# Performance work log

Hardware: AMD Instinct MI355X
Metric: run time of the kernel (lower is better)

Reference implementation:

```python
import jax, jax.numpy as jnp
import numpy as np

B, T, U = 8, 200, 100
D_ENC = D_DEC = J = 512
V = 1024


def setup_inputs() -> dict:
    key = jax.random.key(0)
    ks = jax.random.split(key, 7)
    s = 0.02
    return {
        "enc_out": jax.random.normal(ks[0], (B, T, 1, D_ENC), jnp.float32),
        "dec_out": jax.random.normal(ks[1], (B, 1, U, D_DEC), jnp.float32),
        "W_enc": jax.random.normal(ks[2], (J, D_ENC), jnp.float32) * s,
        "b_enc": jax.random.normal(ks[3], (J,), jnp.float32) * s,
        "W_dec": jax.random.normal(ks[4], (J, D_DEC), jnp.float32) * s,
        "W_out": jax.random.normal(ks[5], (V, J), jnp.float32) * s,
        "b_out": jax.random.normal(ks[6], (V,), jnp.float32) * s,
    }


def reference(enc_out, dec_out, W_enc, b_enc, W_dec, W_out, b_out):
    # lin_enc: (B,T,1,J); lin_dec (no bias): (B,1,U,J)
    enc_proj = jnp.einsum('btod,jd->btoj', enc_out, W_enc) + b_enc
    dec_proj = jnp.einsum('boud,jd->bouj', dec_out, W_dec)
    # broadcast add -> (B,T,U,J), tanh activation
    joint = jnp.tanh(enc_proj + dec_proj)
    # lin_out -> (B,T,U,V)
    return jnp.einsum('btuj,vj->btuv', joint, W_out) + b_out
```

## Files before the change

kernel.cpp:

```cpp
#include <hip/hip_runtime.h>


#define B_ 8
#define T_ 200
#define U_ 100
#define J_ 512
#define V_ 1024
#define M2_ (B_ * T_ * U_)

typedef __attribute__((ext_vector_type(4))) float float4v;
typedef __attribute__((ext_vector_type(8))) short short8;
typedef __attribute__((ext_vector_type(4))) float f32x4;

#define DEV static __device__ __forceinline__

DEV unsigned short f2bf(float f) {
  unsigned int u = __float_as_uint(f);
  u += 0x7FFFu + ((u >> 16) & 1u);
  return (unsigned short)(u >> 16);
}

DEV short8 pack8(float4v a, float4v b) {
  short8 r;
  r[0] = (short)f2bf(a[0]); r[1] = (short)f2bf(a[1]);
  r[2] = (short)f2bf(a[2]); r[3] = (short)f2bf(a[3]);
  r[4] = (short)f2bf(b[0]); r[5] = (short)f2bf(b[1]);
  r[6] = (short)f2bf(b[2]); r[7] = (short)f2bf(b[3]);
  return r;
}

DEV float fast_tanh(float x) {
  float t = __expf(2.0f * x);
  float r = __builtin_amdgcn_rcpf(t + 1.0f);
  return __builtin_fmaf(-2.0f, r, 1.0f);
}

__global__ __launch_bounds__(256) void convert_wout(
    const float* __restrict__ W, unsigned short* __restrict__ Wb) {
  int i = blockIdx.x * 256 + threadIdx.x;
  const float* p = W + (size_t)i * 8;
  float4v a = *(const float4v*)p;
  float4v b = *(const float4v*)(p + 4);
  *(short8*)(Wb + (size_t)i * 8) = pack8(a, b);
}

#define SWZ64(base, row, kb) ((base) + ((row) << 7) + ((((kb) ^ ((row) & 7))) << 4))

__global__ __launch_bounds__(256) void proj_kernel(
    const float* __restrict__ enc_out, const float* __restrict__ dec_out,
    const float* __restrict__ W_enc, const float* __restrict__ b_enc,
    const float* __restrict__ W_dec,
    float* __restrict__ enc_proj, float* __restrict__ dec_proj) {
  __shared__ char lds[16384];
  char* Albs = lds;
  char* Blbs = lds + 8192;

  int bid = blockIdx.x;
  bool is_enc = bid < 200;
  const float* srcA;
  const float* Wsrc;
  float* dst;
  int Mrows, bm, bn;
  if (is_enc) {
    bm = bid >> 3; bn = bid & 7;
    srcA = enc_out; Wsrc = W_enc; dst = enc_proj; Mrows = 1600;
  } else {
    int q = bid - 200;
    bm = q >> 3; bn = q & 7;
    srcA = dec_out; Wsrc = W_dec; dst = dec_proj; Mrows = 800;
  }

  int t = threadIdx.x;
  int l = t & 63;
  int w = t >> 6;
  int wrow = w >> 1, wcol = w & 1;

  f32x4 acc[2][2] = {};

  for (int k0 = 0; k0 < 512; k0 += 64) {
#pragma unroll
    for (int i = 0; i < 2; ++i) {
      int g = t + i * 256;
      int row = g >> 3, kb = g & 7;
      int arow = bm * 64 + row;
      if (arow >= Mrows) arow = Mrows - 1;
      const float* pa = srcA + (size_t)arow * 512 + k0 + kb * 8;
      *(short8*)SWZ64(Albs, row, kb) =
          pack8(*(const float4v*)pa, *(const float4v*)(pa + 4));
      const float* pb = Wsrc + (size_t)(bn * 64 + row) * 512 + k0 + kb * 8;
      *(short8*)SWZ64(Blbs, row, kb) =
          pack8(*(const float4v*)pb, *(const float4v*)(pb + 4));
    }
    __syncthreads();
#pragma unroll
    for (int h = 0; h < 2; ++h) {
      int kb = h * 4 + (l >> 4);
      short8 af[2], bfv[2];
#pragma unroll
      for (int m = 0; m < 2; ++m) {
        int row = wrow * 32 + m * 16 + (l & 15);
        af[m] = *(const short8*)SWZ64(Albs, row, kb);
      }
#pragma unroll
      for (int n = 0; n < 2; ++n) {
        int row = wcol * 32 + n * 16 + (l & 15);
        bfv[n] = *(const short8*)SWZ64(Blbs, row, kb);
      }
#pragma unroll
      for (int m = 0; m < 2; ++m)
#pragma unroll
        for (int n = 0; n < 2; ++n)
          acc[m][n] = __builtin_amdgcn_mfma_f32_16x16x32_bf16(
              af[m], bfv[n], acc[m][n], 0, 0, 0);
    }
    __syncthreads();
  }

#pragma unroll
  for (int n = 0; n < 2; ++n) {
    int col = bn * 64 + wcol * 32 + n * 16 + (l & 15);
    float bias = is_enc ? b_enc[col] : 0.0f;
#pragma unroll
    for (int m = 0; m < 2; ++m) {
#pragma unroll
      for (int j = 0; j < 4; ++j) {
        int gr = bm * 64 + wrow * 32 + m * 16 + (l >> 4) * 4 + j;
        if (gr < Mrows) dst[(size_t)gr * 512 + col] = acc[m][n][j] + bias;
      }
    }
  }
}

__global__ __launch_bounds__(512) void joint_kernel(
    const float* __restrict__ enc_proj, const float* __restrict__ dec_proj,
    const unsigned short* __restrict__ Wb, const float* __restrict__ b_out,
    float* __restrict__ out) {
  __shared__ char lds[163840];
  char* Astrip = lds;
  char* Bbuf0 = lds + 131072;
  char* Bbuf1 = lds + 131072 + 16384;

  int bm = blockIdx.x;
  int t = threadIdx.x;
  int l = t & 63;
  int w = t >> 6;
  int wrow = w >> 2;
  int wcol = w & 3;

  {
#pragma unroll
    for (int i = 0; i < 2; ++i) {
      int g = t + i * 512;
      int rowc = g >> 3;
      int kbp = g & 7;
      int kb = kbp ^ (rowc & 7);
      const unsigned short* src = Wb + (size_t)rowc * 512 + kb * 8;
      __builtin_amdgcn_global_load_lds(
          (const __attribute__((address_space(1))) unsigned int*)src,
          (__attribute__((address_space(3))) unsigned int*)(Bbuf0 + g * 16),
          16, 0, 0);
    }
  }

  {
    int row = t >> 2;
    int gr = bm * 128 + row;
    int b_ = gr / 20000;
    int rem = gr - b_ * 20000;
    int u_ = rem % 100;
    int erow = gr / 100;
    int drow = b_ * 100 + u_;
    const float* pe_base = enc_proj + (size_t)erow * 512;
    const float* pd_base = dec_proj + (size_t)drow * 512;
    char* arow_base = Astrip + row * 1024;
    int swz = row & 7;
#pragma unroll
    for (int i = 0; i < 16; ++i) {
      int kb = i * 4 + (t & 3);
      const float* pe = pe_base + kb * 8;
      const float* pd = pd_base + kb * 8;
      float4v e0 = *(const float4v*)pe;
      float4v e1 = *(const float4v*)(pe + 4);
      float4v d0 = *(const float4v*)pd;
      float4v d1 = *(const float4v*)(pd + 4);
      float4v j0, j1;
#pragma unroll
      for (int q = 0; q < 4; ++q) {
        j0[q] = fast_tanh(e0[q] + d0[q]);
        j1[q] = fast_tanh(e1[q] + d1[q]);
      }
      *(short8*)(arow_base + ((kb ^ swz) << 4)) = pack8(j0, j1);
    }
  }
  __syncthreads();

  f32x4 acc[4][2] = {{{0.f,0.f,0.f,0.f}}};
#pragma unroll
  for (int m = 0; m < 4; ++m)
#pragma unroll
    for (int n = 0; n < 2; ++n)
      acc[m][n] = (f32x4){0.f, 0.f, 0.f, 0.f};

  for (int s = 0; s < 64; ++s) {
    char* Bcur = (s & 1) ? Bbuf1 : Bbuf0;
    char* Bnxt = (s & 1) ? Bbuf0 : Bbuf1;

    if (s < 63) {
      int nt1 = (s + 1) >> 3;
      int k01 = ((s + 1) & 7) * 64;
#pragma unroll
      for (int i = 0; i < 2; ++i) {
        int g = t + i * 512;
        int rowc = g >> 3;
        int kbp = g & 7;
        int kb = kbp ^ (rowc & 7);
        const unsigned short* src =
            Wb + (size_t)(nt1 * 128 + rowc) * 512 + k01 + kb * 8;
        __builtin_amdgcn_global_load_lds(
            (const __attribute__((address_space(1))) unsigned int*)src,
            (__attribute__((address_space(3))) unsigned int*)(Bnxt + g * 16),
            16, 0, 0);
      }
    }

    int k0g = (s & 7) * 8;
#pragma unroll
    for (int kk = 0; kk < 2; ++kk) {
      short8 af[4], bfv[2];
      int kbA = k0g + kk * 4 + (l >> 4);
#pragma unroll
      for (int m = 0; m < 4; ++m) {
        int r = wrow * 64 + m * 16 + (l & 15);
        af[m] = *(const short8*)(Astrip + r * 1024 + (((kbA ^ (r & 7))) << 4));
      }
      int kbB = kk * 4 + (l >> 4);
#pragma unroll
      for (int n = 0; n < 2; ++n) {
        int rc = wcol * 32 + n * 16 + (l & 15);
        bfv[n] = *(const short8*)(Bcur + rc * 128 + (((kbB ^ (rc & 7))) << 4));
      }
      __builtin_amdgcn_s_setprio(1);
#pragma unroll
      for (int m = 0; m < 4; ++m)
#pragma unroll
        for (int n = 0; n < 2; ++n)
          acc[m][n] = __builtin_amdgcn_mfma_f32_16x16x32_bf16(
              af[m], bfv[n], acc[m][n], 0, 0, 0);
      __builtin_amdgcn_s_setprio(0);
    }

    if ((s & 7) == 7) {
      int nt = s >> 3;
#pragma unroll
      for (int n = 0; n < 2; ++n) {
        int col = nt * 128 + wcol * 32 + n * 16 + (l & 15);
        float bias = b_out[col];
#pragma unroll
        for (int m = 0; m < 4; ++m) {
          int r0 = bm * 128 + wrow * 64 + m * 16 + (l >> 4) * 4;
#pragma unroll
          for (int j = 0; j < 4; ++j)
            out[(size_t)(r0 + j) * 1024 + col] = acc[m][n][j] + bias;
          acc[m][n] = (f32x4){0.f, 0.f, 0.f, 0.f};
        }
      }
    }

    __syncthreads();
  }
}

extern "C" void kernel_launch(void* const* d_in, const int* in_sizes, int n_in,
                              void* d_out, int out_size, void* d_ws, size_t ws_size,
                              hipStream_t stream) {
  const float* enc_out = (const float*)d_in[0];
  const float* dec_out = (const float*)d_in[1];
  const float* W_enc   = (const float*)d_in[2];
  const float* b_enc   = (const float*)d_in[3];
  const float* W_dec   = (const float*)d_in[4];
  const float* W_out   = (const float*)d_in[5];
  const float* b_out   = (const float*)d_in[6];
  float* out = (float*)d_out;

  char* ws = (char*)d_ws;
  float* enc_proj = (float*)ws;
  float* dec_proj = (float*)(ws + 3276800);
  unsigned short* Wb = (unsigned short*)(ws + 3276800 + 1638400);

  hipLaunchKernelGGL(convert_wout, dim3(256), dim3(256), 0, stream, W_out, Wb);
  hipLaunchKernelGGL(proj_kernel, dim3(304), dim3(256), 0, stream,
                     enc_out, dec_out, W_enc, b_enc, W_dec, enc_proj, dec_proj);
  hipLaunchKernelGGL(joint_kernel, dim3(M2_ / 128), dim3(512), 0, stream,
                     enc_proj, dec_proj, Wb, b_out, out);
}
```

Baseline: 856.7 us.

## Read W_out fragments directly from global in k-group-major layout, drop LDS B staging

The W_out conversion now writes bf16 weights in a k-group-major layout so each MFMA B fragment is one contiguous 16-byte global load. The joint kernel no longer stages B tiles through double-buffered LDS with per-step barriers. Each wave instead computes a 64x64 tile (4x4 MFMAs) over four column passes, reading B straight from global/L2. The A strip uses an unswizzled k-group-major LDS layout and LDS shrinks to 128KB, with launch_bounds(512,2) added. The intent is to remove barrier and LDS-copy overhead and raise per-wave MFMA density, at the risk of global-load latency stalls and LDS bank conflicts on A reads.

Measured after the change: 839.2 us. -2.0%, faster.

```diff
diff --git a/kernel.cpp b/kernel.cpp
--- a/kernel.cpp
+++ b/kernel.cpp
@@ -36,12 +36,14 @@
 }
 
 __global__ __launch_bounds__(256) void convert_wout(
-    const float* __restrict__ W, unsigned short* __restrict__ Wb) {
+    const float* __restrict__ W, unsigned short* __restrict__ Wbt) {
   int i = blockIdx.x * 256 + threadIdx.x;
-  const float* p = W + (size_t)i * 8;
+  int col = i & 1023;
+  int g = i >> 10;
+  const float* p = W + (size_t)col * 512 + g * 8;
   float4v a = *(const float4v*)p;
   float4v b = *(const float4v*)(p + 4);
-  *(short8*)(Wb + (size_t)i * 8) = pack8(a, b);
+  *(short8*)(Wbt + (size_t)g * 8192 + col * 8) = pack8(a, b);
 }
 
 #define SWZ64(base, row, kb) ((base) + ((row) << 7) + ((((kb) ^ ((row) & 7))) << 4))
@@ -131,14 +133,11 @@
   }
 }
 
-__global__ __launch_bounds__(512) void joint_kernel(
+__global__ __launch_bounds__(512, 2) void joint_kernel(
     const float* __restrict__ enc_proj, const float* __restrict__ dec_proj,
-    const unsigned short* __restrict__ Wb, const float* __restrict__ b_out,
+    const unsigned short* __restrict__ Wbt, const float* __restrict__ b_out,
     float* __restrict__ out) {
-  __shared__ char lds[163840];
-  char* Astrip = lds;
-  char* Bbuf0 = lds + 131072;
-  char* Bbuf1 = lds + 131072 + 16384;
+  __shared__ char As[131072];
 
   int bm = blockIdx.x;
   int t = threadIdx.x;
@@ -146,24 +145,12 @@
   int w = t >> 6;
   int wrow = w >> 2;
   int wcol = w & 3;
+  int lr = l & 15;
+  int lg = l >> 4;
 
   {
-#pragma unroll
-    for (int i = 0; i < 2; ++i) {
-      int g = t + i * 512;
-      int rowc = g >> 3;
-      int kbp = g & 7;
-      int kb = kbp ^ (rowc & 7);
-      const unsigned short* src = Wb + (size_t)rowc * 512 + kb * 8;
-      __builtin_amdgcn_global_load_lds(
-          (const __attribute__((address_space(1))) unsigned int*)src,
-          (__attribute__((address_space(3))) unsigned int*)(Bbuf0 + g * 16),
-          16, 0, 0);
-    }
-  }
-
-  {
-    int row = t >> 2;
+    int row = t & 127;
+    int gbase = t >> 7;
     int gr = bm * 128 + row;
     int b_ = gr / 20000;
     int rem = gr - b_ * 20000;
@@ -172,13 +159,11 @@
     int drow = b_ * 100 + u_;
     const float* pe_base = enc_proj + (size_t)erow * 512;
     const float* pd_base = dec_proj + (size_t)drow * 512;
-    char* arow_base = Astrip + row * 1024;
-    int swz = row & 7;
 #pragma unroll
     for (int i = 0; i < 16; ++i) {
-      int kb = i * 4 + (t & 3);
-      const float* pe = pe_base + kb * 8;
-      const float* pd = pd_base + kb * 8;
+      int g = gbase + i * 4;
+      const float* pe = pe_base + g * 8;
+      const float* pd = pd_base + g * 8;
       float4v e0 = *(const float4v*)pe;
       float4v e1 = *(const float4v*)(pe + 4);
       float4v d0 = *(const float4v*)pd;
@@ -189,84 +174,62 @@
         j0[q] = fast_tanh(e0[q] + d0[q]);
         j1[q] = fast_tanh(e1[q] + d1[q]);
       }
-      *(short8*)(arow_base + ((kb ^ swz) << 4)) = pack8(j0, j1);
+      *(short8*)(As + g * 2048 + row * 16) = pack8(j0, j1);
     }
   }
   __syncthreads();
 
-  f32x4 acc[4][2] = {{{0.f,0.f,0.f,0.f}}};
-#pragma unroll
-  for (int m = 0; m < 4; ++m)
-#pragma unroll
-    for (int n = 0; n < 2; ++n)
-      acc[m][n] = (f32x4){0.f, 0.f, 0.f, 0.f};
-
-  for (int s = 0; s < 64; ++s) {
-    char* Bcur = (s & 1) ? Bbuf1 : Bbuf0;
-    char* Bnxt = (s & 1) ? Bbuf0 : Bbuf1;
-
-    if (s < 63) {
-      int nt1 = (s + 1) >> 3;
-      int k01 = ((s + 1) & 7) * 64;
-#pragma unroll
-      for (int i = 0; i < 2; ++i) {
-        int g = t + i * 512;
-        int rowc = g >> 3;
-        int kbp = g & 7;
-        int kb = kbp ^ (rowc & 7);
-        const unsigned short* src =
-            Wb + (size_t)(nt1 * 128 + rowc) * 512 + k01 + kb * 8;
-        __builtin_amdgcn_global_load_lds(
-            (const __attribute__((address_space(1))) unsigned int*)src,
-            (__attribute__((address_space(3))) unsigned int*)(Bnxt + g * 16),
-            16, 0, 0);
-      }
-    }
-
-    int k0g = (s & 7) * 8;
-#pragma unroll
-    for (int kk = 0; kk < 2; ++kk) {
-      short8 af[4], bfv[2];
-      int kbA = k0g + kk * 4 + (l >> 4);
+  for (int np = 0; np < 4; ++np) {
+    int colbase = np * 256 + wcol * 64;
+    float bias[4];
+#pragma unroll
+    for (int n = 0; n < 4; ++n) bias[n] = b_out[colbase + n * 16 + lr];
+
+    f32x4 acc[4][4];
+#pragma unroll
+    for (int m = 0; m < 4; ++m)
+#pragma unroll
+      for (int n = 0; n < 4; ++n)
+        acc[m][n] = (f32x4){0.f, 0.f, 0.f, 0.f};
+
+#pragma unroll 2
+    for (int ks = 0; ks < 8; ++ks) {
+#pragma unroll
+      for (int kk = 0; kk < 2; ++kk) {
+        int g = ks * 8 + kk * 4 + lg;
+        short8 af[4], bfv[4];
+#pragma unroll
+        for (int n = 0; n < 4; ++n) {
+          int c = colbase + n * 16 + lr;
+          bfv[n] = *(const short8*)(Wbt + (size_t)g * 8192 + c * 8);
+        }
+#pragma unroll
+        for (int m = 0; m < 4; ++m) {
+          int r = wrow * 64 + m * 16 + lr;
+          af[m] = *(const short8*)(As + g * 2048 + r * 16);
+        }
+        __builtin_amdgcn_s_setprio(1);
+#pragma unroll
+        for (int m = 0; m < 4; ++m)
+#pragma unroll
+          for (int n = 0; n < 4; ++n)
+            acc[m][n] = __builtin_amdgcn_mfma_f32_16x16x32_bf16(
+                af[m], bfv[n], acc[m][n], 0, 0, 0);
+        __builtin_amdgcn_s_setprio(0);
+      }
+    }
+
+#pragma unroll
+    for (int n = 0; n < 4; ++n) {
+      int col = colbase + n * 16 + lr;
 #pragma unroll
       for (int m = 0; m < 4; ++m) {
-        int r = wrow * 64 + m * 16 + (l & 15);
-        af[m] = *(const short8*)(Astrip + r * 1024 + (((kbA ^ (r & 7))) << 4));
-      }
-      int kbB = kk * 4 + (l >> 4);
-#pragma unroll
-      for (int n = 0; n < 2; ++n) {
-        int rc = wcol * 32 + n * 16 + (l & 15);
-        bfv[n] = *(const short8*)(Bcur + rc * 128 + (((kbB ^ (rc & 7))) << 4));
-      }
-      __builtin_amdgcn_s_setprio(1);
-#pragma unroll
-      for (int m = 0; m < 4; ++m)
-#pragma unroll
-        for (int n = 0; n < 2; ++n)
-          acc[m][n] = __builtin_amdgcn_mfma_f32_16x16x32_bf16(
-              af[m], bfv[n], acc[m][n], 0, 0, 0);
-      __builtin_amdgcn_s_setprio(0);
-    }
-
-    if ((s & 7) == 7) {
-      int nt = s >> 3;
-#pragma unroll
-      for (int n = 0; n < 2; ++n) {
-        int col = nt * 128 + wcol * 32 + n * 16 + (l & 15);
-        float bias = b_out[col];
-#pragma unroll
-        for (int m = 0; m < 4; ++m) {
-          int r0 = bm * 128 + wrow * 64 + m * 16 + (l >> 4) * 4;
-#pragma unroll
-          for (int j = 0; j < 4; ++j)
-            out[(size_t)(r0 + j) * 1024 + col] = acc[m][n][j] + bias;
-          acc[m][n] = (f32x4){0.f, 0.f, 0.f, 0.f};
-        }
-      }
-    }
-
-    __syncthreads();
+        int r0 = bm * 128 + wrow * 64 + m * 16 + lg * 4;
+#pragma unroll
+        for (int j = 0; j < 4; ++j)
+          out[(size_t)(r0 + j) * 1024 + col] = acc[m][n][j] + bias[n];
+      }
+    }
   }
 }
 
@@ -285,11 +248,11 @@
   char* ws = (char*)d_ws;
   float* enc_proj = (float*)ws;
   float* dec_proj = (float*)(ws + 3276800);
-  unsigned short* Wb = (unsigned short*)(ws + 3276800 + 1638400);
-
-  hipLaunchKernelGGL(convert_wout, dim3(256), dim3(256), 0, stream, W_out, Wb);
+  unsigned short* Wbt = (unsigned short*)(ws + 3276800 + 1638400);
+
+  hipLaunchKernelGGL(convert_wout, dim3(256), dim3(256), 0, stream, W_out, Wbt);
   hipLaunchKernelGGL(proj_kernel, dim3(304), dim3(256), 0, stream,
                      enc_out, dec_out, W_enc, b_enc, W_dec, enc_proj, dec_proj);
   hipLaunchKernelGGL(joint_kernel, dim3(M2_ / 128), dim3(512), 0, stream,
-                     enc_proj, dec_proj, Wb, b_out, out);
-}
+                     enc_proj, dec_proj, Wbt, b_out, out);
+}
```
